# Kernel tuning notes

Measured on AMD Instinct MI355X. Metric: run time of the kernel, lower is better.

The kernel has to match this reference:

```python
import jax, jax.numpy as jnp
import numpy as np

B, T, E, H = 2, 1024, 2048, 32
D = E // H
GROUP = (0.25, 0.25, 0.25, 0.25)
NEG = float(np.finfo(np.float32).min)


def quant_per_token(t, n_bits):
    # smoothquant-style: clamp(absmax, 1e-5) / qmax, per last-dim row
    qmax = 2 ** (n_bits - 1) - 1
    s = jnp.clip(jnp.abs(t).max(-1, keepdims=True), 1e-5, None) / qmax
    return jnp.round(t / s) * s


def w8a8_linear(x, W, b, quant_out=False):
    xq = quant_per_token(x, 8)           # per-token act quant
    Wq = quant_per_token(W, 8)           # per-output-channel weight quant (W: [out, in])
    y = xq @ Wq.T + b
    return quant_per_token(y, 8) if quant_out else y


def to_heads(x):
    # [B, T, E] -> [B*H, T, D]
    return x.reshape(B, T, H, D).transpose(0, 2, 1, 3).reshape(B * H, T, D)


def setup_inputs() -> dict:
    key = jax.random.key(0)
    ks = jax.random.split(key, 9)
    hidden_states = jax.random.normal(ks[0], (B, T, E), jnp.float32)
    causal = jnp.where(jnp.tril(jnp.ones((T, T), bool)), 0.0, NEG).astype(jnp.float32)
    attention_mask = jnp.broadcast_to(causal[None, None], (B, 1, T, T))
    w = 0.02
    return {
        'hidden_states': hidden_states,
        'attention_mask': attention_mask,
        'Wq': jax.random.normal(ks[1], (E, E), jnp.float32) * w,
        'bq': jax.random.normal(ks[2], (E,), jnp.float32) * w,
        'Wk': jax.random.normal(ks[3], (E, E), jnp.float32) * w,
        'bk': jax.random.normal(ks[4], (E,), jnp.float32) * w,
        'Wv': jax.random.normal(ks[5], (E, E), jnp.float32) * w,
        'bv': jax.random.normal(ks[6], (E,), jnp.float32) * w,
        'Wo': jax.random.normal(ks[7], (E, E), jnp.float32) * w,
        'bo': jax.random.normal(ks[8], (E,), jnp.float32) * w,
    }


def reference(hidden_states, attention_mask, Wq, bq, Wk, bk, Wv, bv, Wo, bo):
    scaling = D ** -0.5
    q = w8a8_linear(hidden_states, Wq, bq, quant_out=True) * scaling  # [B,T,E]
    k = w8a8_linear(hidden_states, Wk, bk)                            # [B,T,E]
    v = w8a8_linear(hidden_states, Wv, bv)                            # [B,T,E]

    # ---- heavy-hitter scoring pass (pre-4bit-quant K) ----
    q1, k1 = to_heads(q), to_heads(k)                                 # [BH,T,D]
    aw = jnp.einsum('btd,bsd->bts', q1, k1)                           # [BH,T,T]
    aw = aw.reshape(B, H, T, T) + attention_mask
    aw = jnp.maximum(aw, NEG).reshape(B * H, T, T)
    tmp_attn = jax.nn.softmax(aw, axis=-1)
    acc = tmp_attn.sum(axis=1).sum(axis=0)[None, :]                   # [1,T]
    row_vector = jnp.arange(T, 0, -1).astype(jnp.float32)[None, :]    # T, T-1, ..., 1
    acc = acc / row_vector / (B * H)

    # ---- group-wise top-k heavy-hitter selection ----
    range_size_or = int(T / len(GROUP) / 2)
    start = 1
    idx_list = []
    for i, ratio in enumerate(GROUP):
        rs = int(T * ratio)
        end = min(start + rs - 1, T) if i < len(GROUP) - 1 else T
        partial = acc[:, start - 1:end]
        _, ti = jax.lax.top_k(partial, range_size_or)
        idx_list.append(ti + start - 1)
        start = end + 1
    topk_idx = jnp.concatenate(idx_list, axis=-1).reshape(-1)

    # ---- mixed-precision K quantization ----
    k_abs = jnp.abs(k)
    # fake_quant_mix (8-bit): amax(...)[0] in torch indexes batch 0 -> scales [T,1]
    s_mix = jnp.clip(k_abs.max(-1, keepdims=True)[0] / 127.0, 1e-5, None)  # [T,1]
    k_imp = jnp.round(k / s_mix) * s_mix
    # fake_quant (4-bit, per-row): clamp then divide by 7
    s4 = jnp.clip(k_abs.max(-1, keepdims=True), 1e-5, None) / 7.0
    kq = jnp.round(k / s4) * s4
    kq = kq.at[:, topk_idx, :].set(k_imp[:, topk_idx, :])
    # fake_quant_v (4-bit, per-tensor)
    sv = jnp.clip(jnp.abs(v).max(), 1e-5, None) / 7.0
    vq = jnp.round(v / sv) * sv

    # ---- actual attention with quantized K/V ----
    q2, k2, v2 = to_heads(q), to_heads(kq), to_heads(vq)
    aw2 = jnp.einsum('btd,bsd->bts', q2, k2).reshape(B, H, T, T) + attention_mask
    aw2 = jnp.maximum(aw2, NEG).reshape(B * H, T, T)
    probs = jax.nn.softmax(aw2, axis=-1)
    out = jnp.einsum('bts,bsd->btd', probs, v2)                       # [BH,T,D]
    out = out.reshape(B, H, T, D).transpose(0, 2, 1, 3).reshape(B, T, E)
    return w8a8_linear(out, Wo, bo)
```

## Files before the change

kernel.cpp:

```cpp
#include <hip/hip_runtime.h>
#include <stdint.h>

#define NEG_INF (-__builtin_inff())
#define L2E 1.4426950408889634f

namespace {
constexpr int kT   = 1024;
constexpr int kE   = 2048;
}

using bf16x8 = __attribute__((ext_vector_type(8))) short;
using f32x4  = __attribute__((ext_vector_type(4))) float;
using i32x4  = __attribute__((ext_vector_type(4))) int;
using i32x16 = __attribute__((ext_vector_type(16))) int;

#define MFMA_BF16(a, b, c) __builtin_amdgcn_mfma_f32_16x16x32_bf16((a), (b), (c), 0, 0, 0)
#define MFMA_I8_32(a, b, c) __builtin_amdgcn_mfma_i32_32x32x32_i8((a), (b), (c), 0, 0, 0)

__device__ __forceinline__ void gload16(const void* g, void* l) {
  __builtin_amdgcn_global_load_lds((const __attribute__((address_space(1))) unsigned*)g,
                                   (__attribute__((address_space(3))) unsigned*)l, 16, 0, 0);
}
__device__ __forceinline__ unsigned bfr(float x) {
  unsigned u = __float_as_uint(x);
  return (u + 0x7FFFu + ((u >> 16) & 1u)) >> 16;
}
__device__ __forceinline__ float bf2f(unsigned h) { return __uint_as_float(h << 16); }
__device__ __forceinline__ unsigned pk2(float a, float b) { return bfr(a) | (bfr(b) << 16); }
__device__ __forceinline__ float fexp2(float x) { return __builtin_amdgcn_exp2f(x); }

__device__ __forceinline__ float waveReduceMax(float v) {
#pragma unroll
  for (int o = 32; o > 0; o >>= 1) v = fmaxf(v, __shfl_down(v, o, 64));
  return v;
}
__device__ __forceinline__ float blockMax256(float v, float* r4) {
  const int tid = threadIdx.x;
  float wm = waveReduceMax(v);
  if ((tid & 63) == 0) r4[tid >> 6] = wm;
  __syncthreads();
  float bm = fmaxf(fmaxf(r4[0], r4[1]), fmaxf(r4[2], r4[3]));
  __syncthreads();
  return bm;
}

__global__ __launch_bounds__(256) void k_rowquant_all(const float* __restrict__ Xh,
                                                      const float* __restrict__ W0,
                                                      const float* __restrict__ W1,
                                                      const float* __restrict__ W2,
                                                      const float* __restrict__ W3,
                                                      int8_t* __restrict__ Qh,
                                                      int8_t* __restrict__ Q0,
                                                      int8_t* __restrict__ Q1,
                                                      int8_t* __restrict__ Q2,
                                                      int8_t* __restrict__ Q3,
                                                      float* __restrict__ sX,
                                                      float* __restrict__ sWall,
                                                      unsigned* __restrict__ vmax) {
  const int y = blockIdx.y;
  const float* X = (y == 0) ? Xh : (y == 1) ? W0 : (y == 2) ? W1 : (y == 3) ? W2 : W3;
  int8_t* Qp = (y == 0) ? Qh : (y == 1) ? Q0 : (y == 2) ? Q1 : (y == 3) ? Q2 : Q3;
  const int row = blockIdx.x;
  const int tid = threadIdx.x;
  if (row == 0 && y == 0 && tid == 0) *vmax = 0u;
  const float* x = X + (size_t)row * kE;
  __shared__ float r4[4];
  float am = 0.f;
  float4 v[2];
#pragma unroll
  for (int it = 0; it < 2; ++it) {
    v[it] = *reinterpret_cast<const float4*>(x + (size_t)(it * 256 + tid) * 4);
    am = fmaxf(am, fmaxf(fmaxf(fabsf(v[it].x), fabsf(v[it].y)), fmaxf(fabsf(v[it].z), fabsf(v[it].w))));
  }
  const float bm = blockMax256(am, r4);
  const float s = fmaxf(bm, 1e-5f) / 127.f;
  int8_t* xq = Qp + (size_t)row * kE;
#pragma unroll
  for (int it = 0; it < 2; ++it) {
    const int i = (it * 256 + tid) * 4;
    char4 q;
    q.x = (char)(int)rintf(v[it].x / s);
    q.y = (char)(int)rintf(v[it].y / s);
    q.z = (char)(int)rintf(v[it].z / s);
    q.w = (char)(int)rintf(v[it].w / s);
    *reinterpret_cast<char4*>(xq + i) = q;
  }
  if (tid == 0) {
    if (y == 0) sX[row] = s;
    else sWall[(y - 1) * kE + row] = s;
  }
}

__global__ __launch_bounds__(256) void k_rowquant_i8(const float* __restrict__ X,
                                                     int8_t* __restrict__ Xq,
                                                     float* __restrict__ S) {
  const int row = blockIdx.x;
  const int tid = threadIdx.x;
  const float* x = X + (size_t)row * kE;
  __shared__ float r4[4];
  float am = 0.f;
  float4 v[2];
#pragma unroll
  for (int it = 0; it < 2; ++it) {
    v[it] = *reinterpret_cast<const float4*>(x + (size_t)(it * 256 + tid) * 4);
    am = fmaxf(am, fmaxf(fmaxf(fabsf(v[it].x), fabsf(v[it].y)), fmaxf(fabsf(v[it].z), fabsf(v[it].w))));
  }
  const float bm = blockMax256(am, r4);
  const float s = fmaxf(bm, 1e-5f) / 127.f;
  int8_t* xq = Xq + (size_t)row * kE;
#pragma unroll
  for (int it = 0; it < 2; ++it) {
    const int i = (it * 256 + tid) * 4;
    char4 q;
    q.x = (char)(int)rintf(v[it].x / s);
    q.y = (char)(int)rintf(v[it].y / s);
    q.z = (char)(int)rintf(v[it].z / s);
    q.w = (char)(int)rintf(v[it].w / s);
    *reinterpret_cast<char4*>(xq + i) = q;
  }
  if (tid == 0) S[row] = s;
}

__global__ __launch_bounds__(256) void k_prep(const float* __restrict__ Qb,
                                              const float* __restrict__ Kb,
                                              const float* __restrict__ Vb,
                                              short* __restrict__ qi,
                                              float* __restrict__ sqg,
                                              short* __restrict__ khi,
                                              short* __restrict__ klo,
                                              float* __restrict__ s4,
                                              float* __restrict__ smix,
                                              unsigned* __restrict__ vmax) {
  const int row = blockIdx.x;
  const int tid = threadIdx.x;
  __shared__ float r4[4];

  {
    const float* x = Qb + (size_t)row * kE;
    float am = 0.f;
    float4 v[2];
#pragma unroll
    for (int it = 0; it < 2; ++it) {
      v[it] = *reinterpret_cast<const float4*>(x + (size_t)(it * 256 + tid) * 4);
      am = fmaxf(am, fmaxf(fmaxf(fabsf(v[it].x), fabsf(v[it].y)), fmaxf(fabsf(v[it].z), fabsf(v[it].w))));
    }
    const float bm = blockMax256(am, r4);
    const float s = fmaxf(bm, 1e-5f) / 127.f;
#pragma unroll
    for (int it = 0; it < 2; ++it) {
      const int i = (it * 256 + tid) * 4;
      short4 q;
      q.x = (short)bfr(rintf(v[it].x / s));
      q.y = (short)bfr(rintf(v[it].y / s));
      q.z = (short)bfr(rintf(v[it].z / s));
      q.w = (short)bfr(rintf(v[it].w / s));
      *reinterpret_cast<short4*>(qi + (size_t)row * kE + i) = q;
    }
    if (tid == 0) sqg[row] = s * 0.125f;
  }

  {
    const float* x = Kb + (size_t)row * kE;
    float am = 0.f;
    float4 v[2];
#pragma unroll
    for (int it = 0; it < 2; ++it) {
      v[it] = *reinterpret_cast<const float4*>(x + (size_t)(it * 256 + tid) * 4);
      am = fmaxf(am, fmaxf(fmaxf(fabsf(v[it].x), fabsf(v[it].y)), fmaxf(fabsf(v[it].z), fabsf(v[it].w))));
    }
    const float bm = blockMax256(am, r4);
#pragma unroll
    for (int it = 0; it < 2; ++it) {
      const int i = (it * 256 + tid) * 4;
      short4 hh, ll;
      unsigned hb;
      hb = bfr(v[it].x); hh.x = (short)hb; ll.x = (short)bfr(v[it].x - bf2f(hb));
      hb = bfr(v[it].y); hh.y = (short)hb; ll.y = (short)bfr(v[it].y - bf2f(hb));
      hb = bfr(v[it].z); hh.z = (short)hb; ll.z = (short)bfr(v[it].z - bf2f(hb));
      hb = bfr(v[it].w); hh.w = (short)hb; ll.w = (short)bfr(v[it].w - bf2f(hb));
      *reinterpret_cast<short4*>(khi + (size_t)row * kE + i) = hh;
      *reinterpret_cast<short4*>(klo + (size_t)row * kE + i) = ll;
    }
    if (tid == 0) {
      s4[row] = fmaxf(bm, 1e-5f) / 7.f;
      if (row < kT) smix[row] = fmaxf(bm / 127.f, 1e-5f);
    }
  }

  {
    const float* x = Vb + (size_t)row * kE;
    float am = 0.f;
#pragma unroll
    for (int it = 0; it < 2; ++it) {
      const float4 v = *reinterpret_cast<const float4*>(x + (size_t)(it * 256 + tid) * 4);
      am = fmaxf(am, fmaxf(fmaxf(fabsf(v.x), fabsf(v.y)), fmaxf(fabsf(v.z), fabsf(v.w))));
    }
    const float bm = blockMax256(am, r4);
    if (tid == 0) atomicMax(vmax, __float_as_uint(bm));
  }
}

__global__ __launch_bounds__(256) void k_kvint(const float* __restrict__ Kb,
                                               const float* __restrict__ s4,
                                               const float* __restrict__ smix,
                                               const int* __restrict__ sel,
                                               short* __restrict__ ki,
                                               float* __restrict__ skg,
                                               const float* __restrict__ Vb,
                                               const unsigned* __restrict__ vmax,
                                               short* __restrict__ vt) {
  const int bid = blockIdx.x;
  const int tid = threadIdx.x;
  if (bid < 2048) {
    const int row = bid;
    const int t = row & (kT - 1);
    const float s = sel[t] ? smix[t] : s4[row];
    const float* x = Kb + (size_t)row * kE;
#pragma unroll
    for (int it = 0; it < 2; ++it) {
      const int i = (it * 256 + tid) * 4;
      const float4 v = *reinterpret_cast<const float4*>(x + i);
      short4 q;
      q.x = (short)bfr(rintf(v.x / s));
      q.y = (short)bfr(rintf(v.y / s));
      q.z = (short)bfr(rintf(v.z / s));
      q.w = (short)bfr(rintf(v.w / s));
      *reinterpret_cast<short4*>(ki + (size_t)row * kE + i) = q;
    }
    if (tid == 0) skg[row] = s;
  } else {
    const int t = bid - 2048;
    const int tt = t & 15, bh = t >> 4;
    const int b = bh >> 5, h = bh & 31;
    const float sv = fmaxf(__uint_as_float(*vmax), 1e-5f) / 7.f;
    __shared__ short tr[64][80];
#pragma unroll
    for (int i = 0; i < 4; ++i) {
      const int e = i * 256 + tid;
      const int tok = e >> 4, d4 = (e & 15) * 4;
      const float4 v = *reinterpret_cast<const float4*>(
          &Vb[(size_t)(b * kT + tt * 64 + tok) * kE + h * 64 + d4]);
      tr[d4 + 0][tok] = (short)bfr(rintf(v.x / sv));
      tr[d4 + 1][tok] = (short)bfr(rintf(v.y / sv));
      tr[d4 + 2][tok] = (short)bfr(rintf(v.z / sv));
      tr[d4 + 3][tok] = (short)bfr(rintf(v.w / sv));
    }
    __syncthreads();
#pragma unroll
    for (int i = 0; i < 2; ++i) {
      const int e = i * 256 + tid;
      const int d = e >> 3, u = e & 7;
      const bf16x8 row = *reinterpret_cast<const bf16x8*>(&tr[d][u * 8]);
      *reinterpret_cast<bf16x8*>(&vt[(size_t)(bh * 64 + d) * kT + tt * 64 + u * 8]) = row;
    }
  }
}

__device__ __forceinline__ void gemm_i8_body(int m0, int n0,
                                             const int8_t* __restrict__ A,
                                             const float* __restrict__ sa,
                                             const int8_t* __restrict__ Bw,
                                             const float* __restrict__ sw,
                                             const float* __restrict__ bias,
                                             float* __restrict__ Y,
                                             int8_t* AsBase, int8_t* BsBase) {
  const int tid = threadIdx.x;
  const int lane = tid & 63, w = tid >> 6;
  const int l31 = lane & 31, lh = lane >> 5;
  const int wmRow = (w >> 1) * 64, wnRow = (w & 1) * 64;

  const i32x16 zero16 = {0};
  i32x16 acc00 = zero16, acc01 = zero16, acc10 = zero16, acc11 = zero16;

  auto stage = [&](int buf, int k0) {
    int8_t* As = AsBase + buf * 16384;
    int8_t* Bs = BsBase + buf * 8192;
#pragma unroll
    for (int i = 0; i < 2; ++i) {
      const int s = tid + i * 512;
      const int row = s >> 2, gp = s & 3;
      const int gs = gp ^ ((row >> 1) & 3);
      gload16(A + (size_t)(m0 + row) * kE + k0 + gs * 16, As + s * 16);
    }
    {
      const int row = tid >> 2, gp = tid & 3;
      const int gs = gp ^ ((row >> 1) & 3);
      gload16(Bw + (size_t)(n0 + row) * kE + k0 + gs * 16, Bs + tid * 16);
    }
  };

  stage(0, 0);
  __syncthreads();
  int cur = 0;

  const int ar0 = wmRow + l31, ar1 = wmRow + 32 + l31;
  const int br0 = wnRow + l31, br1 = wnRow + 32 + l31;
  const int sa0 = (ar0 >> 1) & 3, sa1 = (ar1 >> 1) & 3;
  const int sb0 = (br0 >> 1) & 3, sb1 = (br1 >> 1) & 3;

  for (int k0 = 0; k0 < kE; k0 += 64) {
    if (k0 + 64 < kE) stage(cur ^ 1, k0 + 64);
    const int8_t* As = AsBase + cur * 16384;
    const int8_t* Bs = BsBase + cur * 8192;
#pragma unroll
    for (int j = 0; j < 2; ++j) {
      const int gn = lh + 2 * j;
      const i32x4 a0 = *reinterpret_cast<const i32x4*>(As + ((ar0 << 2) + (gn ^ sa0)) * 16);
      const i32x4 a1 = *reinterpret_cast<const i32x4*>(As + ((ar1 << 2) + (gn ^ sa1)) * 16);
      const i32x4 b0 = *reinterpret_cast<const i32x4*>(Bs + ((br0 << 2) + (gn ^ sb0)) * 16);
      const i32x4 b1 = *reinterpret_cast<const i32x4*>(Bs + ((br1 << 2) + (gn ^ sb1)) * 16);
      acc00 = MFMA_I8_32(a0, b0, acc00);
      acc01 = MFMA_I8_32(a0, b1, acc01);
      acc10 = MFMA_I8_32(a1, b0, acc10);
      acc11 = MFMA_I8_32(a1, b1, acc11);
    }
    __syncthreads();
    cur ^= 1;
  }

#pragma unroll
  for (int fn = 0; fn < 2; ++fn) {
    const int col = n0 + wnRow + fn * 32 + l31;
    const float swn = sw[col], bn = bias[col];
#pragma unroll
    for (int fm = 0; fm < 2; ++fm) {
      const i32x16 accv = (fm == 0) ? ((fn == 0) ? acc00 : acc01)
                                    : ((fn == 0) ? acc10 : acc11);
      const int r0 = m0 + wmRow + fm * 32 + 4 * lh;
#pragma unroll
      for (int reg = 0; reg < 16; ++reg) {
        const int row = r0 + (reg & 3) + 8 * (reg >> 2);
        Y[(size_t)row * kE + col] = (float)accv[reg] * sa[row] * swn + bn;
      }
    }
  }
}

__global__ __launch_bounds__(512) void k_gemm_i8(const int8_t* __restrict__ A,
                                                 const float* __restrict__ sa,
                                                 const int8_t* __restrict__ Bw,
                                                 const float* __restrict__ sw,
                                                 const float* __restrict__ bias,
                                                 float* __restrict__ Y) {
  __shared__ int8_t As[2 * 16384];
  __shared__ int8_t Bs[2 * 8192];
  const int linear = blockIdx.x + (blockIdx.y << 4);
  const int nid = (linear & 7) * 16 + (linear >> 3);
  const int x = nid & 15, y = nid >> 4;
  gemm_i8_body(y * 256, x * 128, A, sa, Bw, sw, bias, Y, As, Bs);
}

__global__ __launch_bounds__(512) void k_gemm_qkv(const int8_t* __restrict__ A,
                                                  const float* __restrict__ sa,
                                                  const int8_t* __restrict__ Wq,
                                                  const int8_t* __restrict__ Wk,
                                                  const int8_t* __restrict__ Wv,
                                                  const float* __restrict__ sWall,
                                                  const float* __restrict__ bq,
                                                  const float* __restrict__ bk,
                                                  const float* __restrict__ bv,
                                                  float* __restrict__ qb,
                                                  float* __restrict__ kb,
                                                  float* __restrict__ vb) {
  __shared__ int8_t As[2 * 16384];
  __shared__ int8_t Bs[2 * 8192];
  const int linear = blockIdx.x + (blockIdx.y << 4) + (blockIdx.z << 7);
  const int nid = (linear & 7) * 48 + (linear >> 3);
  const int x = nid & 15, y = (nid >> 4) & 7, z = nid >> 7;
  const int8_t* Bw = (z == 0) ? Wq : (z == 1) ? Wk : Wv;
  const float* sw = sWall + (size_t)z * kE;
  const float* bias = (z == 0) ? bq : (z == 1) ? bk : bv;
  float* Y = (z == 0) ? qb : (z == 1) ? kb : vb;
  gemm_i8_body(y * 256, x * 128, A, sa, Bw, sw, bias, Y, As, Bs);
}

__global__ __launch_bounds__(256) void k_attn1(const short* __restrict__ qi,
                                               const short* __restrict__ khi,
                                               const short* __restrict__ klo,
                                               const float* __restrict__ sqg,
                                               float* __restrict__ accPart) {
  const int r1 = blockIdx.x, r2 = 15 - r1, bh = blockIdx.y;
  const int b = bh >> 5, h = bh & 31;
  const int tid = threadIdx.x, lane = tid & 63, w = tid >> 6;
  const int g = lane >> 4, c16 = lane & 15;
  const int swz = c16 & 7;

  __shared__ short qs1[64 * 64];
  __shared__ short qs2[64 * 64];
  __shared__ short hbuf[2][64 * 64];
  __shared__ short lbuf[2][64 * 64];
  __shared__ float accL[1024];
  __shared__ float Arow[128], Crow[128];

  for (int i = tid; i < 1024; i += 256) accL[i] = 0.f;

  const int st8 = tid >> 3, su = tid & 7;
  {
    const int tokb1 = b * kT + r1 * 64;
    const int tokb2 = b * kT + r2 * 64;
#pragma unroll
    for (int i = 0; i < 2; ++i) {
      const int tok = i * 32 + st8;
      const int co = ((su ^ (tok & 7)) << 3);
      gload16(qi + (size_t)(tokb1 + tok) * kE + h * 64 + co, &qs1[tok * 64 + su * 8]);
      gload16(qi + (size_t)(tokb2 + tok) * kE + h * 64 + co, &qs2[tok * 64 + su * 8]);
    }
  }
  auto stage = [&](int buf, int kt) {
    const int tokb = b * kT + kt * 64;
#pragma unroll
    for (int i = 0; i < 2; ++i) {
      const int tok = i * 32 + st8;
      const size_t gsrc = (size_t)(tokb + tok) * kE + h * 64 + ((su ^ (tok & 7)) << 3);
      gload16(khi + gsrc, &hbuf[buf][tok * 64 + su * 8]);
      gload16(klo + gsrc, &lbuf[buf][tok * 64 + su * 8]);
    }
  };

  stage(0, 0);
  __syncthreads();

  const int qrow = w * 16 + c16;
  const bf16x8 q1_0 = *reinterpret_cast<const bf16x8*>(&qs1[qrow * 64 + ((g ^ swz) << 3)]);
  const bf16x8 q1_1 = *reinterpret_cast<const bf16x8*>(&qs1[qrow * 64 + (((4 + g) ^ swz) << 3)]);
  const bf16x8 q2_0 = *reinterpret_cast<const bf16x8*>(&qs2[qrow * 64 + ((g ^ swz) << 3)]);
  const bf16x8 q2_1 = *reinterpret_cast<const bf16x8*>(&qs2[qrow * 64 + (((4 + g) ^ swz) << 3)]);
  const float A1c = sqg[b * kT + r1 * 64 + qrow] * L2E;
  const float A2c = sqg[b * kT + r2 * 64 + qrow] * L2E;

  float m1 = NEG_INF, l1 = 0.f, m2_ = NEG_INF, l2 = 0.f;
  int cur = 0;

  for (int kt = 0; kt <= r2; ++kt) {
    if (kt < r2) stage(cur ^ 1, kt + 1);
    const bool act1 = kt <= r1;
    float p1[4][4], p2[4][4];
    float pm1 = NEG_INF, pm2 = NEG_INF;
    __builtin_amdgcn_s_setprio(1);
#pragma unroll
    for (int f = 0; f < 4; ++f) {
      const int tokl = f * 16 + c16;
      const bf16x8 ah0 = *reinterpret_cast<const bf16x8*>(&hbuf[cur][tokl * 64 + ((g ^ swz) << 3)]);
      const bf16x8 ah1 = *reinterpret_cast<const bf16x8*>(&hbuf[cur][tokl * 64 + (((4 + g) ^ swz) << 3)]);
      const bf16x8 al0 = *reinterpret_cast<const bf16x8*>(&lbuf[cur][tokl * 64 + ((g ^ swz) << 3)]);
      const bf16x8 al1 = *reinterpret_cast<const bf16x8*>(&lbuf[cur][tokl * 64 + (((4 + g) ^ swz) << 3)]);
      f32x4 sB = {0.f, 0.f, 0.f, 0.f};
      sB = MFMA_BF16(ah0, q2_0, sB);
      sB = MFMA_BF16(ah1, q2_1, sB);
      sB = MFMA_BF16(al0, q2_0, sB);
      sB = MFMA_BF16(al1, q2_1, sB);
      f32x4 sA = {0.f, 0.f, 0.f, 0.f};
      if (act1) {
        sA = MFMA_BF16(ah0, q1_0, sA);
        sA = MFMA_BF16(ah1, q1_1, sA);
        sA = MFMA_BF16(al0, q1_0, sA);
        sA = MFMA_BF16(al1, q1_1, sA);
      }
#pragma unroll
      for (int r = 0; r < 4; ++r) {
        const int tokd = f * 16 + g * 4 + r;
        float s2 = sB[r] * A2c;
        if (kt == r2 && tokd > qrow) s2 = NEG_INF;
        p2[f][r] = s2;
        pm2 = fmaxf(pm2, s2);
        float s1 = sA[r] * A1c;
        if (kt == r1 && tokd > qrow) s1 = NEG_INF;
        p1[f][r] = s1;
        pm1 = fmaxf(pm1, s1);
      }
    }
    __builtin_amdgcn_s_setprio(0);
    {
      pm2 = fmaxf(pm2, __shfl_xor(pm2, 16));
      pm2 = fmaxf(pm2, __shfl_xor(pm2, 32));
      const bool upd = pm2 > m2_ + 8.f;
      const float mn = upd ? fmaxf(m2_, pm2) : m2_;
      const float fsc = fexp2(m2_ - mn);
      float rs = 0.f;
#pragma unroll
      for (int f = 0; f < 4; ++f)
#pragma unroll
        for (int r = 0; r < 4; ++r) rs += fexp2(p2[f][r] - mn);
      rs += __shfl_xor(rs, 16);
      rs += __shfl_xor(rs, 32);
      l2 = l2 * fsc + rs;
      m2_ = mn;
    }
    if (act1) {
      pm1 = fmaxf(pm1, __shfl_xor(pm1, 16));
      pm1 = fmaxf(pm1, __shfl_xor(pm1, 32));
      const bool upd = pm1 > m1 + 8.f;
      const float mn = upd ? fmaxf(m1, pm1) : m1;
      const float fsc = fexp2(m1 - mn);
      float rs = 0.f;
#pragma unroll
      for (int f = 0; f < 4; ++f)
#pragma unroll
        for (int r = 0; r < 4; ++r) rs += fexp2(p1[f][r] - mn);
      rs += __shfl_xor(rs, 16);
      rs += __shfl_xor(rs, 32);
      l1 = l1 * fsc + rs;
      m1 = mn;
    }
    __syncthreads();
    cur ^= 1;
  }

  if (g == 0) {
    Arow[qrow] = A1c;
    Crow[qrow] = -(m1 + __builtin_amdgcn_logf(l1));
    Arow[64 + qrow] = A2c;
    Crow[64 + qrow] = -(m2_ + __builtin_amdgcn_logf(l2));
  }
  stage(0, 0);
  __syncthreads();

  bf16x8 qa1_0[4], qa1_1[4], qa2_0[4], qa2_1[4];
  float Ar1[4][4], Cr1[4][4], Ar2[4][4], Cr2[4][4];
#pragma unroll
  for (int f = 0; f < 4; ++f) {
    const int qr = f * 16 + c16;
    qa1_0[f] = *reinterpret_cast<const bf16x8*>(&qs1[qr * 64 + ((g ^ swz) << 3)]);
    qa1_1[f] = *reinterpret_cast<const bf16x8*>(&qs1[qr * 64 + (((4 + g) ^ swz) << 3)]);
    qa2_0[f] = *reinterpret_cast<const bf16x8*>(&qs2[qr * 64 + ((g ^ swz) << 3)]);
    qa2_1[f] = *reinterpret_cast<const bf16x8*>(&qs2[qr * 64 + (((4 + g) ^ swz) << 3)]);
#pragma unroll
    for (int r = 0; r < 4; ++r) {
      const int tokd = f * 16 + g * 4 + r;
      Ar1[f][r] = Arow[tokd];
      Cr1[f][r] = Crow[tokd];
      Ar2[f][r] = Arow[64 + tokd];
      Cr2[f][r] = Crow[64 + tokd];
    }
  }

  const int ktokL = w * 16 + c16;
  cur = 0;
  for (int kt = 0; kt <= r2; ++kt) {
    if (kt < r2) stage(cur ^ 1, kt + 1);
    const bf16x8 kh0 = *reinterpret_cast<const bf16x8*>(&hbuf[cur][ktokL * 64 + ((g ^ swz) << 3)]);
    const bf16x8 kh1 = *reinterpret_cast<const bf16x8*>(&hbuf[cur][ktokL * 64 + (((4 + g) ^ swz) << 3)]);
    const bf16x8 kl0 = *reinterpret_cast<const bf16x8*>(&lbuf[cur][ktokL * 64 + ((g ^ swz) << 3)]);
    const bf16x8 kl1 = *reinterpret_cast<const bf16x8*>(&lbuf[cur][ktokL * 64 + (((4 + g) ^ swz) << 3)]);
    float csum = 0.f;
    __builtin_amdgcn_s_setprio(1);
    if (kt < r2) {
#pragma unroll
      for (int f = 0; f < 4; ++f) {
        f32x4 sf = {0.f, 0.f, 0.f, 0.f};
        sf = MFMA_BF16(qa2_0[f], kh0, sf);
        sf = MFMA_BF16(qa2_1[f], kh1, sf);
        sf = MFMA_BF16(qa2_0[f], kl0, sf);
        sf = MFMA_BF16(qa2_1[f], kl1, sf);
#pragma unroll
        for (int r = 0; r < 4; ++r) csum += fexp2(fmaf(sf[r], Ar2[f][r], Cr2[f][r]));
      }
    } else {
#pragma unroll
      for (int f = 0; f < 4; ++f) {
        f32x4 sf = {0.f, 0.f, 0.f, 0.f};
        sf = MFMA_BF16(qa2_0[f], kh0, sf);
        sf = MFMA_BF16(qa2_1[f], kh1, sf);
        sf = MFMA_BF16(qa2_0[f], kl0, sf);
        sf = MFMA_BF16(qa2_1[f], kl1, sf);
#pragma unroll
        for (int r = 0; r < 4; ++r) {
          const float v = fexp2(fmaf(sf[r], Ar2[f][r], Cr2[f][r]));
          if (ktokL <= (f * 16 + g * 4 + r)) csum += v;
        }
      }
    }
    if (kt <= r1) {
      if (kt < r1) {
#pragma unroll
        for (int f = 0; f < 4; ++f) {
          f32x4 sf = {0.f, 0.f, 0.f, 0.f};
          sf = MFMA_BF16(qa1_0[f], kh0, sf);
          sf = MFMA_BF16(qa1_1[f], kh1, sf);
          sf = MFMA_BF16(qa1_0[f], kl0, sf);
          sf = MFMA_BF16(qa1_1[f], kl1, sf);
#pragma unroll
          for (int r = 0; r < 4; ++r) csum += fexp2(fmaf(sf[r], Ar1[f][r], Cr1[f][r]));
        }
      } else {
#pragma unroll
        for (int f = 0; f < 4; ++f) {
          f32x4 sf = {0.f, 0.f, 0.f, 0.f};
          sf = MFMA_BF16(qa1_0[f], kh0, sf);
          sf = MFMA_BF16(qa1_1[f], kh1, sf);
          sf = MFMA_BF16(qa1_0[f], kl0, sf);
          sf = MFMA_BF16(qa1_1[f], kl1, sf);
#pragma unroll
          for (int r = 0; r < 4; ++r) {
            const float v = fexp2(fmaf(sf[r], Ar1[f][r], Cr1[f][r]));
            if (ktokL <= (f * 16 + g * 4 + r)) csum += v;
          }
        }
      }
    }
    __builtin_amdgcn_s_setprio(0);
    csum += __shfl_xor(csum, 16);
    csum += __shfl_xor(csum, 32);
    if (g == 0) accL[kt * 64 + ktokL] += csum;
    __syncthreads();
    cur ^= 1;
  }

  for (int i = tid; i < 1024; i += 256)
    accPart[(size_t)(bh * 8 + r1) * 1024 + i] = accL[i];
}

__global__ __launch_bounds__(256) void k_acctopk(const float* __restrict__ part,
                                                 int* __restrict__ sel) {
  const int i = threadIdx.x;
  const int j = blockIdx.x * 256 + i;
  float s = 0.f;
  for (int p = 0; p < 512; ++p) s += part[(size_t)p * 1024 + j];
  const float vi = s / (float)(kT - j) / 64.f;
  __shared__ float v[256];
  v[i] = vi;
  __syncthreads();
  int rank = 0;
  for (int jj = 0; jj < 256; ++jj) {
    const float vj = v[jj];
    rank += (vj > vi) || (vj == vi && jj < i);
  }
  sel[j] = (rank < 128) ? 1 : 0;
}

__global__ __launch_bounds__(256) void k_attn2(const short* __restrict__ qi,
                                               const short* __restrict__ ki,
                                               const short* __restrict__ vt,
                                               const float* __restrict__ sqg,
                                               const float* __restrict__ skg,
                                               const unsigned* __restrict__ vmax,
                                               float* __restrict__ ctx) {
  const int r1 = blockIdx.x, r2 = 15 - r1, bh = blockIdx.y;
  const int b = bh >> 5, h = bh & 31;
  const int tid = threadIdx.x, lane = tid & 63, w = tid >> 6;
  const int g = lane >> 4, c16 = lane & 15;
  const int swz = c16 & 7;
  const int wrow = w * 16 + c16;

  __shared__ short kbuf[2][64 * 64];
  __shared__ short vbuf[2][64 * 64];
  __shared__ float skl[2][64];

  const int qtokA = b * kT + r1 * 64 + wrow;
  const int qtokB = b * kT + r2 * 64 + wrow;
  bf16x8 qfA[2], qfB[2];
  qfA[0] = *reinterpret_cast<const bf16x8*>(qi + (size_t)qtokA * kE + h * 64 + g * 8);
  qfA[1] = *reinterpret_cast<const bf16x8*>(qi + (size_t)qtokA * kE + h * 64 + 32 + g * 8);
  qfB[0] = *reinterpret_cast<const bf16x8*>(qi + (size_t)qtokB * kE + h * 64 + g * 8);
  qfB[1] = *reinterpret_cast<const bf16x8*>(qi + (size_t)qtokB * kE + h * 64 + 32 + g * 8);
  const float sqA = sqg[qtokA] * L2E;
  const float sqB = sqg[qtokB] * L2E;
  const float sv = fmaxf(__uint_as_float(*vmax), 1e-5f) / 7.f;

  const int st8 = tid >> 3, su = tid & 7;
  auto stage = [&](int buf, int kt) {
    const int tokb = b * kT + kt * 64;
#pragma unroll
    for (int i = 0; i < 2; ++i) {
      const int tok = i * 32 + st8;
      gload16(ki + (size_t)(tokb + tok) * kE + h * 64 + ((su ^ (tok & 7)) << 3),
              &kbuf[buf][tok * 64 + su * 8]);
      gload16(vt + (size_t)(bh * 64 + tok) * kT + kt * 64 + ((su ^ (tok & 7)) << 3),
              &vbuf[buf][tok * 64 + su * 8]);
    }
    if (tid < 64) skl[buf][tid] = skg[tokb + tid];
  };

  float mA = NEG_INF, lA = 0.f, mB = NEG_INF, lB = 0.f;
  f32x4 otA[4], otB[4];
#pragma unroll
  for (int f = 0; f < 4; ++f) {
    otA[f] = (f32x4){0.f, 0.f, 0.f, 0.f};
    otB[f] = (f32x4){0.f, 0.f, 0.f, 0.f};
  }

  stage(0, 0);
  __syncthreads();
  int cur = 0;

  const int srcLo = c16 | ((g & 1) << 5);
  const int srcHi = srcLo | 16;
  const bool selq = ((g >> 1) & 1) != 0;

  for (int kt = 0; kt <= r2; ++kt) {
    if (kt < r2) stage(cur ^ 1, kt + 1);
    const bool act1 = kt <= r1;

    f32x4 sfB4[4], sfA4[4];
    __builtin_amdgcn_s_setprio(1);
#pragma unroll
    for (int f = 0; f < 4; ++f) {
      const int tokl = f * 16 + c16;
      const bf16x8 k0 = *reinterpret_cast<const bf16x8*>(&kbuf[cur][tokl * 64 + ((g ^ swz) << 3)]);
      const bf16x8 k1 = *reinterpret_cast<const bf16x8*>(&kbuf[cur][tokl * 64 + (((4 + g) ^ swz) << 3)]);
      f32x4 s = {0.f, 0.f, 0.f, 0.f};
      s = MFMA_BF16(k0, qfB[0], s);
      s = MFMA_BF16(k1, qfB[1], s);
      sfB4[f] = s;
      f32x4 sa = {0.f, 0.f, 0.f, 0.f};
      if (act1) {
        sa = MFMA_BF16(k0, qfA[0], sa);
        sa = MFMA_BF16(k1, qfA[1], sa);
      }
      sfA4[f] = sa;
    }
    __builtin_amdgcn_s_setprio(0);

    {
      float p[4][4];
      float pm = NEG_INF;
#pragma unroll
      for (int f = 0; f < 4; ++f)
#pragma unroll
        for (int r = 0; r < 4; ++r) {
          const int tokd = f * 16 + g * 4 + r;
          float s2 = sfB4[f][r] * skl[cur][tokd] * sqB;
          if (kt == r2 && tokd > wrow) s2 = NEG_INF;
          p[f][r] = s2;
          pm = fmaxf(pm, s2);
        }
      pm = fmaxf(pm, __shfl_xor(pm, 16));
      pm = fmaxf(pm, __shfl_xor(pm, 32));
      const bool upd = pm > mB + 8.f;
      const float mn = upd ? fmaxf(mB, pm) : mB;
      const float fsc = fexp2(mB - mn);
      mB = mn;
      float rs = 0.f;
#pragma unroll
      for (int f = 0; f < 4; ++f)
#pragma unroll
        for (int r = 0; r < 4; ++r) {
          const float e = fexp2(p[f][r] - mn);
          p[f][r] = e;
          rs += e;
        }
      rs += __shfl_xor(rs, 16);
      rs += __shfl_xor(rs, 32);
      lB = lB * fsc + rs;
      if (__any(upd)) {
#pragma unroll
        for (int f = 0; f < 4; ++f)
#pragma unroll
          for (int r = 0; r < 4; ++r) otB[f][r] *= fsc;
      }
#pragma unroll
      for (int c = 0; c < 2; ++c) {
        const unsigned q0a = pk2(p[2 * c][0], p[2 * c][1]);
        const unsigned q0b = pk2(p[2 * c][2], p[2 * c][3]);
        const unsigned q1a = pk2(p[2 * c + 1][0], p[2 * c + 1][1]);
        const unsigned q1b = pk2(p[2 * c + 1][2], p[2 * c + 1][3]);
        unsigned a0, a1;
        union { unsigned u[4]; bf16x8 v; } Bh;
        a0 = __shfl(q0a, srcLo); a1 = __shfl(q1a, srcLo); Bh.u[0] = selq ? a1 : a0;
        a0 = __shfl(q0b, srcLo); a1 = __shfl(q1b, srcLo); Bh.u[1] = selq ? a1 : a0;
        a0 = __shfl(q0a, srcHi); a1 = __shfl(q1a, srcHi); Bh.u[2] = selq ? a1 : a0;
        a0 = __shfl(q0b, srcHi); a1 = __shfl(q1b, srcHi); Bh.u[3] = selq ? a1 : a0;
        __builtin_amdgcn_s_setprio(1);
#pragma unroll
        for (int fd = 0; fd < 4; ++fd) {
          const int d = fd * 16 + c16;
          const bf16x8 va = *reinterpret_cast<const bf16x8*>(
              &vbuf[cur][d * 64 + ((((c << 2) | g) ^ swz) << 3)]);
          otB[fd] = MFMA_BF16(va, Bh.v, otB[fd]);
        }
        __builtin_amdgcn_s_setprio(0);
      }
    }

    if (act1) {
      float p[4][4];
      float pm = NEG_INF;
#pragma unroll
      for (int f = 0; f < 4; ++f)
#pragma unroll
        for (int r = 0; r < 4; ++r) {
          const int tokd = f * 16 + g * 4 + r;
          float s2 = sfA4[f][r] * skl[cur][tokd] * sqA;
          if (kt == r1 && tokd > wrow) s2 = NEG_INF;
          p[f][r] = s2;
          pm = fmaxf(pm, s2);
        }
      pm = fmaxf(pm, __shfl_xor(pm, 16));
      pm = fmaxf(pm, __shfl_xor(pm, 32));
      const bool upd = pm > mA + 8.f;
      const float mn = upd ? fmaxf(mA, pm) : mA;
      const float fsc = fexp2(mA - mn);
      mA = mn;
      float rs = 0.f;
#pragma unroll
      for (int f = 0; f < 4; ++f)
#pragma unroll
        for (int r = 0; r < 4; ++r) {
          const float e = fexp2(p[f][r] - mn);
          p[f][r] = e;
          rs += e;
        }
      rs += __shfl_xor(rs, 16);
      rs += __shfl_xor(rs, 32);
      lA = lA * fsc + rs;
      if (__any(upd)) {
#pragma unroll
        for (int f = 0; f < 4; ++f)
#pragma unroll
          for (int r = 0; r < 4; ++r) otA[f][r] *= fsc;
      }
#pragma unroll
      for (int c = 0; c < 2; ++c) {
        const unsigned q0a = pk2(p[2 * c][0], p[2 * c][1]);
        const unsigned q0b = pk2(p[2 * c][2], p[2 * c][3]);
        const unsigned q1a = pk2(p[2 * c + 1][0], p[2 * c + 1][1]);
        const unsigned q1b = pk2(p[2 * c + 1][2], p[2 * c + 1][3]);
        unsigned a0, a1;
        union { unsigned u[4]; bf16x8 v; } Bh;
        a0 = __shfl(q0a, srcLo); a1 = __shfl(q1a, srcLo); Bh.u[0] = selq ? a1 : a0;
        a0 = __shfl(q0b, srcLo); a1 = __shfl(q1b, srcLo); Bh.u[1] = selq ? a1 : a0;
        a0 = __shfl(q0a, srcHi); a1 = __shfl(q1a, srcHi); Bh.u[2] = selq ? a1 : a0;
        a0 = __shfl(q0b, srcHi); a1 = __shfl(q1b, srcHi); Bh.u[3] = selq ? a1 : a0;
        __builtin_amdgcn_s_setprio(1);
#pragma unroll
        for (int fd = 0; fd < 4; ++fd) {
          const int d = fd * 16 + c16;
          const bf16x8 va = *reinterpret_cast<const bf16x8*>(
              &vbuf[cur][d * 64 + ((((c << 2) | g) ^ swz) << 3)]);
          otA[fd] = MFMA_BF16(va, Bh.v, otA[fd]);
        }
        __builtin_amdgcn_s_setprio(0);
      }
    }

    __syncthreads();
    cur ^= 1;
  }

  const float ilA = sv / lA;
  const float ilB = sv / lB;
#pragma unroll
  for (int fd = 0; fd < 4; ++fd) {
    float4 oA, oB;
    oA.x = otA[fd][0] * ilA; oA.y = otA[fd][1] * ilA;
    oA.z = otA[fd][2] * ilA; oA.w = otA[fd][3] * ilA;
    oB.x = otB[fd][0] * ilB; oB.y = otB[fd][1] * ilB;
    oB.z = otB[fd][2] * ilB; oB.w = otB[fd][3] * ilB;
    *reinterpret_cast<float4*>(&ctx[(size_t)qtokA * kE + h * 64 + fd * 16 + g * 4]) = oA;
    *reinterpret_cast<float4*>(&ctx[(size_t)qtokB * kE + h * 64 + fd * 16 + g * 4]) = oB;
  }
}

extern "C" void kernel_launch(void* const* d_in, const int* in_sizes, int n_in,
                              void* d_out, int out_size, void* d_ws, size_t ws_size,
                              hipStream_t stream) {
  (void)in_sizes; (void)n_in; (void)out_size; (void)ws_size;
  const float* hs = (const float*)d_in[0];
  const float* Wq = (const float*)d_in[2];
  const float* bq = (const float*)d_in[3];
  const float* Wk = (const float*)d_in[4];
  const float* bk = (const float*)d_in[5];
  const float* Wv = (const float*)d_in[6];
  const float* bv = (const float*)d_in[7];
  const float* Wo = (const float*)d_in[8];
  const float* bo = (const float*)d_in[9];
  float* out = (float*)d_out;

  char* p = (char*)d_ws;
  auto take = [&](size_t bytes) {
    char* r = p;
    p += (bytes + 255) & ~(size_t)255;
    return r;
  };
  float* qb  = (float*)take((size_t)2048 * 2048 * 4);
  float* kb  = (float*)take((size_t)2048 * 2048 * 4);
  float* vb  = (float*)take((size_t)2048 * 2048 * 4);
  float* ctx = (float*)take((size_t)2048 * 2048 * 4);
  short* qiB = (short*)take((size_t)2048 * 2048 * 2);
  int8_t* xq  = (int8_t*)take((size_t)2048 * 2048);
  int8_t* woq = (int8_t*)take((size_t)2048 * 2048);
  float* sX    = (float*)take(2048 * 4);
  float* sWall = (float*)take(4 * 2048 * 4);
  float* sC    = (float*)take(2048 * 4);
  float* s4v   = (float*)take(2048 * 4);
  float* smix  = (float*)take(1024 * 4);
  int*   sel   = (int*)take(1024 * 4);
  float* sqg   = (float*)take(2048 * 4);
  float* skg   = (float*)take(2048 * 4);
  unsigned* vmax = (unsigned*)take(256);

  short* khi = (short*)qb;
  short* klo = (short*)qb + (size_t)2048 * 2048;
  short* kint = khi;
  short* vtp  = klo;
  float* accPart = ctx;
  int8_t* wqq = (int8_t*)ctx + ((size_t)2 << 20);
  int8_t* wkq = (int8_t*)ctx + ((size_t)6 << 20);
  int8_t* wvq = (int8_t*)ctx + ((size_t)10 << 20);
  int8_t* cq = xq;

  k_rowquant_all<<<dim3(2048, 5), 256, 0, stream>>>(hs, Wq, Wk, Wv, Wo,
                                                    xq, wqq, wkq, wvq, woq,
                                                    sX, sWall, vmax);

  k_gemm_qkv<<<dim3(16, 8, 3), 512, 0, stream>>>(xq, sX, wqq, wkq, wvq, sWall,
                                                 bq, bk, bv, qb, kb, vb);

  k_prep<<<2048, 256, 0, stream>>>(qb, kb, vb, qiB, sqg, khi, klo, s4v, smix, vmax);

  k_attn1<<<dim3(8, 64), 256, 0, stream>>>(qiB, khi, klo, sqg, accPart);
  k_acctopk<<<4, 256, 0, stream>>>(accPart, sel);

  k_kvint<<<3072, 256, 0, stream>>>(kb, s4v, smix, sel, kint, skg, vb, vmax, vtp);

  k_attn2<<<dim3(8, 64), 256, 0, stream>>>(qiB, kint, vtp, sqg, skg, vmax, ctx);

  k_rowquant_i8<<<2048, 256, 0, stream>>>(ctx, cq, sC);
  k_gemm_i8<<<dim3(16, 8), 512, 0, stream>>>(cq, sC, woq, sWall + 3 * 2048, bo, out);
}
```

Baseline: 239.6 us.

## Retile int8 GEMMs to 128x128 with triple-buffered LDS prefetch; drop setprio in attention

The int8 GEMM body moves from 256x128 tiles with 512 threads to 128x128 tiles with 256 threads. It now uses a three-stage LDS ring that prefetches two K-steps ahead, replacing full __syncthreads with explicit vmcnt/lgkmcnt waits and a bare barrier. The QKV and output-projection launch grids double in block count to match, and the tile swizzle is updated. Separately, all s_setprio hints are removed from the attention kernels. The aim is to hide global-load latency better and raise occupancy, at the cost of reloading A and B tiles more often per output element.

```diff
diff --git a/kernel.cpp b/kernel.cpp
--- a/kernel.cpp
+++ b/kernel.cpp
@@ -267,41 +267,47 @@
   const int tid = threadIdx.x;
   const int lane = tid & 63, w = tid >> 6;
   const int l31 = lane & 31, lh = lane >> 5;
-  const int wmRow = (w >> 1) * 64, wnRow = (w & 1) * 64;
+  const int wm = (w >> 1) * 64, wn = (w & 1) * 64;
 
   const i32x16 zero16 = {0};
   i32x16 acc00 = zero16, acc01 = zero16, acc10 = zero16, acc11 = zero16;
 
   auto stage = [&](int buf, int k0) {
-    int8_t* As = AsBase + buf * 16384;
+    int8_t* As = AsBase + buf * 8192;
     int8_t* Bs = BsBase + buf * 8192;
 #pragma unroll
     for (int i = 0; i < 2; ++i) {
-      const int s = tid + i * 512;
+      const int s = i * 256 + tid;
       const int row = s >> 2, gp = s & 3;
       const int gs = gp ^ ((row >> 1) & 3);
       gload16(A + (size_t)(m0 + row) * kE + k0 + gs * 16, As + s * 16);
     }
-    {
-      const int row = tid >> 2, gp = tid & 3;
+#pragma unroll
+    for (int i = 0; i < 2; ++i) {
+      const int s = i * 256 + tid;
+      const int row = s >> 2, gp = s & 3;
       const int gs = gp ^ ((row >> 1) & 3);
-      gload16(Bw + (size_t)(n0 + row) * kE + k0 + gs * 16, Bs + tid * 16);
+      gload16(Bw + (size_t)(n0 + row) * kE + k0 + gs * 16, Bs + s * 16);
     }
   };
 
+  const int NT = kE / 64;
   stage(0, 0);
-  __syncthreads();
-  int cur = 0;
-
-  const int ar0 = wmRow + l31, ar1 = wmRow + 32 + l31;
-  const int br0 = wnRow + l31, br1 = wnRow + 32 + l31;
+  stage(1, 64);
+  asm volatile("s_waitcnt vmcnt(4)" ::: "memory");
+  __builtin_amdgcn_s_barrier();
+
+  const int ar0 = wm + l31, ar1 = wm + 32 + l31;
+  const int br0 = wn + l31, br1 = wn + 32 + l31;
   const int sa0 = (ar0 >> 1) & 3, sa1 = (ar1 >> 1) & 3;
   const int sb0 = (br0 >> 1) & 3, sb1 = (br1 >> 1) & 3;
 
-  for (int k0 = 0; k0 < kE; k0 += 64) {
-    if (k0 + 64 < kE) stage(cur ^ 1, k0 + 64);
-    const int8_t* As = AsBase + cur * 16384;
-    const int8_t* Bs = BsBase + cur * 8192;
+  int buf = 0, nbuf = 2;
+  for (int t = 0; t < NT; ++t) {
+    const bool pf = (t + 2 < NT);
+    if (pf) stage(nbuf, (t + 2) * 64);
+    const int8_t* As = AsBase + buf * 8192;
+    const int8_t* Bs = BsBase + buf * 8192;
 #pragma unroll
     for (int j = 0; j < 2; ++j) {
       const int gn = lh + 2 * j;
@@ -314,19 +320,26 @@
       acc10 = MFMA_I8_32(a1, b0, acc10);
       acc11 = MFMA_I8_32(a1, b1, acc11);
     }
-    __syncthreads();
-    cur ^= 1;
+    asm volatile("s_waitcnt lgkmcnt(0)" ::: "memory");
+    if (pf) {
+      asm volatile("s_waitcnt vmcnt(4)" ::: "memory");
+    } else {
+      asm volatile("s_waitcnt vmcnt(0)" ::: "memory");
+    }
+    __builtin_amdgcn_s_barrier();
+    buf = (buf == 2) ? 0 : buf + 1;
+    nbuf = (nbuf == 2) ? 0 : nbuf + 1;
   }
 
 #pragma unroll
   for (int fn = 0; fn < 2; ++fn) {
-    const int col = n0 + wnRow + fn * 32 + l31;
+    const int col = n0 + wn + fn * 32 + l31;
     const float swn = sw[col], bn = bias[col];
 #pragma unroll
     for (int fm = 0; fm < 2; ++fm) {
       const i32x16 accv = (fm == 0) ? ((fn == 0) ? acc00 : acc01)
                                     : ((fn == 0) ? acc10 : acc11);
-      const int r0 = m0 + wmRow + fm * 32 + 4 * lh;
+      const int r0 = m0 + wm + fm * 32 + 4 * lh;
 #pragma unroll
       for (int reg = 0; reg < 16; ++reg) {
         const int row = r0 + (reg & 3) + 8 * (reg >> 2);
@@ -336,21 +349,21 @@
   }
 }
 
-__global__ __launch_bounds__(512) void k_gemm_i8(const int8_t* __restrict__ A,
+__global__ __launch_bounds__(256) void k_gemm_i8(const int8_t* __restrict__ A,
                                                  const float* __restrict__ sa,
                                                  const int8_t* __restrict__ Bw,
                                                  const float* __restrict__ sw,
                                                  const float* __restrict__ bias,
                                                  float* __restrict__ Y) {
-  __shared__ int8_t As[2 * 16384];
-  __shared__ int8_t Bs[2 * 8192];
+  __shared__ int8_t As[3 * 8192];
+  __shared__ int8_t Bs[3 * 8192];
   const int linear = blockIdx.x + (blockIdx.y << 4);
-  const int nid = (linear & 7) * 16 + (linear >> 3);
+  const int nid = (linear & 7) * 32 + (linear >> 3);
   const int x = nid & 15, y = nid >> 4;
-  gemm_i8_body(y * 256, x * 128, A, sa, Bw, sw, bias, Y, As, Bs);
-}
-
-__global__ __launch_bounds__(512) void k_gemm_qkv(const int8_t* __restrict__ A,
+  gemm_i8_body(y * 128, x * 128, A, sa, Bw, sw, bias, Y, As, Bs);
+}
+
+__global__ __launch_bounds__(256) void k_gemm_qkv(const int8_t* __restrict__ A,
                                                   const float* __restrict__ sa,
                                                   const int8_t* __restrict__ Wq,
                                                   const int8_t* __restrict__ Wk,
@@ -362,16 +375,16 @@
                                                   float* __restrict__ qb,
                                                   float* __restrict__ kb,
                                                   float* __restrict__ vb) {
-  __shared__ int8_t As[2 * 16384];
-  __shared__ int8_t Bs[2 * 8192];
-  const int linear = blockIdx.x + (blockIdx.y << 4) + (blockIdx.z << 7);
-  const int nid = (linear & 7) * 48 + (linear >> 3);
-  const int x = nid & 15, y = (nid >> 4) & 7, z = nid >> 7;
+  __shared__ int8_t As[3 * 8192];
+  __shared__ int8_t Bs[3 * 8192];
+  const int linear = blockIdx.x + (blockIdx.y << 4) + (blockIdx.z << 8);
+  const int nid = (linear & 7) * 96 + (linear >> 3);
+  const int x = nid & 15, y = (nid >> 4) & 15, z = nid >> 8;
   const int8_t* Bw = (z == 0) ? Wq : (z == 1) ? Wk : Wv;
   const float* sw = sWall + (size_t)z * kE;
   const float* bias = (z == 0) ? bq : (z == 1) ? bk : bv;
   float* Y = (z == 0) ? qb : (z == 1) ? kb : vb;
-  gemm_i8_body(y * 256, x * 128, A, sa, Bw, sw, bias, Y, As, Bs);
+  gemm_i8_body(y * 128, x * 128, A, sa, Bw, sw, bias, Y, As, Bs);
 }
 
 __global__ __launch_bounds__(256) void k_attn1(const short* __restrict__ qi,
@@ -436,7 +449,6 @@
     const bool act1 = kt <= r1;
     float p1[4][4], p2[4][4];
     float pm1 = NEG_INF, pm2 = NEG_INF;
-    __builtin_amdgcn_s_setprio(1);
 #pragma unroll
     for (int f = 0; f < 4; ++f) {
       const int tokl = f * 16 + c16;
@@ -469,7 +481,6 @@
         pm1 = fmaxf(pm1, s1);
       }
     }
-    __builtin_amdgcn_s_setprio(0);
     {
       pm2 = fmaxf(pm2, __shfl_xor(pm2, 16));
       pm2 = fmaxf(pm2, __shfl_xor(pm2, 32));
@@ -543,7 +554,6 @@
     const bf16x8 kl0 = *reinterpret_cast<const bf16x8*>(&lbuf[cur][ktokL * 64 + ((g ^ swz) << 3)]);
     const bf16x8 kl1 = *reinterpret_cast<const bf16x8*>(&lbuf[cur][ktokL * 64 + (((4 + g) ^ swz) << 3)]);
     float csum = 0.f;
-    __builtin_amdgcn_s_setprio(1);
     if (kt < r2) {
 #pragma unroll
       for (int f = 0; f < 4; ++f) {
@@ -598,7 +608,6 @@
         }
       }
     }
-    __builtin_amdgcn_s_setprio(0);
     csum += __shfl_xor(csum, 16);
     csum += __shfl_xor(csum, 32);
     if (g == 0) accL[kt * 64 + ktokL] += csum;
@@ -692,7 +701,6 @@
     const bool act1 = kt <= r1;
 
     f32x4 sfB4[4], sfA4[4];
-    __builtin_amdgcn_s_setprio(1);
 #pragma unroll
     for (int f = 0; f < 4; ++f) {
       const int tokl = f * 16 + c16;
@@ -709,7 +717,6 @@
       }
       sfA4[f] = sa;
     }
-    __builtin_amdgcn_s_setprio(0);
 
     {
       float p[4][4];
@@ -760,7 +767,6 @@
         a0 = __shfl(q0b, srcLo); a1 = __shfl(q1b, srcLo); Bh.u[1] = selq ? a1 : a0;
         a0 = __shfl(q0a, srcHi); a1 = __shfl(q1a, srcHi); Bh.u[2] = selq ? a1 : a0;
         a0 = __shfl(q0b, srcHi); a1 = __shfl(q1b, srcHi); Bh.u[3] = selq ? a1 : a0;
-        __builtin_amdgcn_s_setprio(1);
 #pragma unroll
         for (int fd = 0; fd < 4; ++fd) {
           const int d = fd * 16 + c16;
@@ -768,7 +774,6 @@
               &vbuf[cur][d * 64 + ((((c << 2) | g) ^ swz) << 3)]);
           otB[fd] = MFMA_BF16(va, Bh.v, otB[fd]);
         }
-        __builtin_amdgcn_s_setprio(0);
       }
     }
 
@@ -821,7 +826,6 @@
         a0 = __shfl(q0b, srcLo); a1 = __shfl(q1b, srcLo); Bh.u[1] = selq ? a1 : a0;
         a0 = __shfl(q0a, srcHi); a1 = __shfl(q1a, srcHi); Bh.u[2] = selq ? a1 : a0;
         a0 = __shfl(q0b, srcHi); a1 = __shfl(q1b, srcHi); Bh.u[3] = selq ? a1 : a0;
-        __builtin_amdgcn_s_setprio(1);
 #pragma unroll
         for (int fd = 0; fd < 4; ++fd) {
           const int d = fd * 16 + c16;
@@ -829,7 +833,6 @@
               &vbuf[cur][d * 64 + ((((c << 2) | g) ^ swz) << 3)]);
           otA[fd] = MFMA_BF16(va, Bh.v, otA[fd]);
         }
-        __builtin_amdgcn_s_setprio(0);
       }
     }
 
@@ -903,8 +906,8 @@
                                                     xq, wqq, wkq, wvq, woq,
                                                     sX, sWall, vmax);
 
-  k_gemm_qkv<<<dim3(16, 8, 3), 512, 0, stream>>>(xq, sX, wqq, wkq, wvq, sWall,
-                                                 bq, bk, bv, qb, kb, vb);
+  k_gemm_qkv<<<dim3(16, 16, 3), 256, 0, stream>>>(xq, sX, wqq, wkq, wvq, sWall,
+                                                  bq, bk, bv, qb, kb, vb);
 
   k_prep<<<2048, 256, 0, stream>>>(qb, kb, vb, qiB, sqg, khi, klo, s4v, smix, vmax);
 
@@ -916,5 +919,5 @@
   k_attn2<<<dim3(8, 64), 256, 0, stream>>>(qiB, kint, vtp, sqg, skg, vmax, ctx);
 
   k_rowquant_i8<<<2048, 256, 0, stream>>>(ctx, cq, sC);
-  k_gemm_i8<<<dim3(16, 8), 512, 0, stream>>>(cq, sC, woq, sWall + 3 * 2048, bo, out);
-}
+  k_gemm_i8<<<dim3(16, 16), 256, 0, stream>>>(cq, sC, woq, sWall + 3 * 2048, bo, out);
+}
```

Result: slower. 252.1 us (+5.2%).
